# Kernel optimization log

Hardware: AMD Instinct MI355X
Metric: run time of the kernel (lower is better)

Reference implementation:

```python
import jax, jax.numpy as jnp
import numpy as np

N_ROWS = 500000   # entities (rows of P)
D = 128           # factor dim
B = 4096          # batch of i indices
K = 64            # fixed neighbor degree (n_repeat in original code)


def setup_inputs() -> dict:
    key = jax.random.key(0)
    k1, k2, k3, k4 = jax.random.split(key, 4)
    P = jax.random.uniform(k1, (N_ROWS, D), dtype=jnp.float32)
    i_indices = jax.random.randint(k2, (B,), 0, N_ROWS, dtype=jnp.int64 if jax.config.jax_enable_x64 else jnp.int32)
    j_indices = jax.random.randint(k3, (B, K), 0, N_ROWS, dtype=jnp.int64 if jax.config.jax_enable_x64 else jnp.int32)
    S_vals = jax.random.uniform(k4, (B, K), dtype=jnp.float32)
    return {"P": P, "i_indices": i_indices, "j_indices": j_indices, "S_vals": S_vals}


def reference(P, i_indices, j_indices, S_vals):
    # similarity_matrix_penalty (entity=True):
    # penalty = sum_{b, k} S[i_b, j_{b,k}] * || P[i_b] - P[j_{b,k}] ||_2
    Pi = P[i_indices][:, None, :]          # [B, 1, D]
    Pj = P[j_indices]                      # [B, K, D]
    diff = Pi - Pj                         # [B, K, D]
    norms = jnp.sqrt(jnp.sum(diff * diff, axis=-1))  # [B, K], torch.norm(p=2, dim=1)
    penalty = jnp.sum(norms * S_vals)
    return penalty
```

## Files before the change

### kernel.cpp

```cpp
#include <hip/hip_runtime.h>

#define DIMS 128
#define KNBR 64

__global__ __launch_bounds__(256) void penalty_partial_kernel(
    const float* __restrict__ P,
    const int*   __restrict__ iIdx,
    const int*   __restrict__ jIdx,
    const float* __restrict__ S,
    float*       __restrict__ ws)
{
    const int b    = blockIdx.x;
    const int lane = threadIdx.x & 63;
    const int wave = threadIdx.x >> 6;

    const int i = iIdx[b];
    const float2 pi = *reinterpret_cast<const float2*>(P + (size_t)i * DIMS + lane * 2);

    int   js[16];
    float ss[16];
    #pragma unroll
    for (int u = 0; u < 16; ++u) {
        const int k = wave + 4 * u;
        js[u] = jIdx[b * KNBR + k];
        ss[u] = S[b * KNBR + k];
    }

    float acc = 0.0f;
    #pragma unroll
    for (int u = 0; u < 16; ++u) {
        const float2 pj = *reinterpret_cast<const float2*>(P + (size_t)js[u] * DIMS + lane * 2);
        const float dx = pi.x - pj.x;
        const float dy = pi.y - pj.y;
        float sq = dx * dx + dy * dy;
        #pragma unroll
        for (int off = 32; off > 0; off >>= 1)
            sq += __shfl_xor(sq, off, 64);
        acc += sqrtf(sq) * ss[u];
    }

    __shared__ float partial[4];
    if (lane == 0) partial[wave] = acc;
    __syncthreads();
    if (threadIdx.x == 0)
        ws[b] = partial[0] + partial[1] + partial[2] + partial[3];
}

__global__ __launch_bounds__(256) void reduce_kernel(
    const float* __restrict__ ws, float* __restrict__ out, int n)
{
    const int t = threadIdx.x;
    float acc = 0.0f;
    for (int idx = t; idx < n; idx += 256)
        acc += ws[idx];

    #pragma unroll
    for (int off = 32; off > 0; off >>= 1)
        acc += __shfl_xor(acc, off, 64);

    __shared__ float partial[4];
    if ((t & 63) == 0) partial[t >> 6] = acc;
    __syncthreads();
    if (t == 0)
        out[0] = partial[0] + partial[1] + partial[2] + partial[3];
}

extern "C" void kernel_launch(void* const* d_in, const int* in_sizes, int n_in,
                              void* d_out, int out_size, void* d_ws, size_t ws_size,
                              hipStream_t stream) {
    const float* P    = (const float*)d_in[0];
    const int*   iIdx = (const int*)d_in[1];
    const int*   jIdx = (const int*)d_in[2];
    const float* S    = (const float*)d_in[3];
    float*       out  = (float*)d_out;
    float*       ws   = (float*)d_ws;

    const int B = in_sizes[1];

    penalty_partial_kernel<<<B, 256, 0, stream>>>(P, iIdx, jIdx, S, ws);
    reduce_kernel<<<1, 256, 0, stream>>>(ws, out, B);
}
```

Baseline: 320.9 us.

## Split waves into 16-lane groups to gather four neighbor rows at once

Each 64-lane wave is split into four 16-lane subgroups. Each subgroup handles one neighbor row using two float4 loads per lane, so a wave works on four neighbors at a time instead of one. All eight row loads per lane are issued before any arithmetic, which keeps more gathers in flight and cuts the per-neighbor shuffle reduction from six steps to four. The per-subgroup accumulators are replicated across lanes, so a full-wave reduction follows, scaled by 1/16 to undo the duplication. This adds register pressure and a small change in floating-point summation order.

```diff
diff --git a/kernel.cpp b/kernel.cpp
--- a/kernel.cpp
+++ b/kernel.cpp
@@ -13,34 +13,56 @@
     const int b    = blockIdx.x;
     const int lane = threadIdx.x & 63;
     const int wave = threadIdx.x >> 6;
+    const int sub  = lane >> 4;
+    const int t    = lane & 15;
 
-    const int i = iIdx[b];
-    const float2 pi = *reinterpret_cast<const float2*>(P + (size_t)i * DIMS + lane * 2);
+    const float* Pi = P + (size_t)iIdx[b] * DIMS;
+    const float4 pi0 = *reinterpret_cast<const float4*>(Pi + t * 4);
+    const float4 pi1 = *reinterpret_cast<const float4*>(Pi + 64 + t * 4);
 
-    int   js[16];
-    float ss[16];
+    const int kbase = b * KNBR + wave * 16 + sub;
+    int   js[4];
+    float sv[4];
     #pragma unroll
-    for (int u = 0; u < 16; ++u) {
-        const int k = wave + 4 * u;
-        js[u] = jIdx[b * KNBR + k];
-        ss[u] = S[b * KNBR + k];
+    for (int g = 0; g < 4; ++g) {
+        js[g] = jIdx[kbase + g * 4];
+        sv[g] = S[kbase + g * 4];
+    }
+
+    float4 pj0[4], pj1[4];
+    #pragma unroll
+    for (int g = 0; g < 4; ++g) {
+        const float* Pj = P + (size_t)js[g] * DIMS;
+        pj0[g] = *reinterpret_cast<const float4*>(Pj + t * 4);
+        pj1[g] = *reinterpret_cast<const float4*>(Pj + 64 + t * 4);
     }
 
     float acc = 0.0f;
     #pragma unroll
-    for (int u = 0; u < 16; ++u) {
-        const float2 pj = *reinterpret_cast<const float2*>(P + (size_t)js[u] * DIMS + lane * 2);
-        const float dx = pi.x - pj.x;
-        const float dy = pi.y - pj.y;
-        float sq = dx * dx + dy * dy;
-        #pragma unroll
-        for (int off = 32; off > 0; off >>= 1)
-            sq += __shfl_xor(sq, off, 64);
-        acc += sqrtf(sq) * ss[u];
+    for (int g = 0; g < 4; ++g) {
+        float d0 = pi0.x - pj0[g].x;
+        float d1 = pi0.y - pj0[g].y;
+        float d2 = pi0.z - pj0[g].z;
+        float d3 = pi0.w - pj0[g].w;
+        float d4 = pi1.x - pj1[g].x;
+        float d5 = pi1.y - pj1[g].y;
+        float d6 = pi1.z - pj1[g].z;
+        float d7 = pi1.w - pj1[g].w;
+        float sq = d0*d0 + d1*d1 + d2*d2 + d3*d3
+                 + d4*d4 + d5*d5 + d6*d6 + d7*d7;
+        sq += __shfl_xor(sq, 1, 64);
+        sq += __shfl_xor(sq, 2, 64);
+        sq += __shfl_xor(sq, 4, 64);
+        sq += __shfl_xor(sq, 8, 64);
+        acc += sqrtf(sq) * sv[g];
     }
 
+    #pragma unroll
+    for (int off = 32; off > 0; off >>= 1)
+        acc += __shfl_xor(acc, off, 64);
+
     __shared__ float partial[4];
-    if (lane == 0) partial[wave] = acc;
+    if (lane == 0) partial[wave] = acc * 0.0625f;
     __syncthreads();
     if (threadIdx.x == 0)
         ws[b] = partial[0] + partial[1] + partial[2] + partial[3];
```

Measured after the change: 319.0 us. Within noise of the previous version (-0.6%).
